# Performance work log

Hardware: AMD Instinct MI355X
Metric: run time of the kernel (lower is better)

## Reference

```python
import jax, jax.numpy as jnp
import numpy as np

N = 100_000          # nodes
E = 3_200_000        # edges (avg degree 32)
H = 20               # hidden_channels (node feature width, = 10 one-hot + 10 mlp)
EH = 64              # edge_hidden_dim
EO = 10              # edge_output_dim
THRESHOLD = 1.0


def setup_inputs() -> dict:
    key = jax.random.key(0)
    ks = jax.random.split(key, 12)
    x = jax.random.normal(ks[0], (N, 2, H), dtype=jnp.float32)
    edge_index = jax.random.randint(ks[1], (2, E), 0, N, dtype=jnp.int32)
    # distances strictly in (0, threshold]
    edge_attr = jax.random.uniform(ks[2], (E, 1), jnp.float32, 1e-4, THRESHOLD)
    # parameters (torch.rand init as in the module)
    a = jax.random.uniform(ks[3], (1,), jnp.float32)
    b = jax.random.uniform(ks[4], (1,), jnp.float32) + 1.0
    gamma1 = jax.random.uniform(ks[5], (H, H), jnp.float32)
    gamma2 = jax.random.uniform(ks[6], (H, H), jnp.float32)
    bias = jax.random.uniform(ks[7], (H,), jnp.float32)
    # edge MLP: Linear(1, EH) -> ReLU -> Linear(EH, EO)
    W1 = jax.random.normal(ks[8], (1, EH), jnp.float32)
    b1 = jnp.zeros((EH,), jnp.float32)
    W2 = jax.random.normal(ks[9], (EH, EO), jnp.float32) / np.sqrt(EH)
    b2 = jnp.zeros((EO,), jnp.float32)
    return dict(x=x, edge_index=edge_index, edge_attr=edge_attr, a=a, b=b,
                gamma1=gamma1, gamma2=gamma2, bias=bias, W1=W1, b1=b1, W2=W2, b2=b2)


def reference(x, edge_index, edge_attr, a, b, gamma1, gamma2, bias, W1, b1, W2, b2):
    src, dst = edge_index[0], edge_index[1]
    # --- edge features ---
    h = jax.nn.relu(edge_attr @ W1 + b1)            # [E, EH]
    mlp_out = h @ W2 + b2                           # [E, EO]
    # one-hot distance bucket: 10 equal intervals over (0, threshold], idx 10 -> 9
    idx = jnp.clip((edge_attr[:, 0] * (10.0 / THRESHOLD)).astype(jnp.int32), 0, 9)
    one_hot = jax.nn.one_hot(idx, 10, dtype=x.dtype)  # [E, 10]
    eac = jnp.concatenate([one_hot, mlp_out], axis=1)  # edge_attr_combined [E, 20]
    # --- per-source-node normalization (w_tilde) ---
    sum_w = jax.ops.segment_sum(eac, src, num_segments=N)  # [N, 20]
    sw = sum_w[src]                                        # [E, 20]
    safe = jnp.where(sw != 0, sw, 1.0)
    w_tilde = jnp.where(sw != 0, eac / safe, jnp.asarray(0.01, x.dtype))
    # --- rho weighting on node features ---
    h_j = x[src, 0]                                  # [E, 20]
    h_jp = x[dst, 0]                                 # [E, 20]
    rho = jnp.abs(a * h_j - (1.0 - a) * h_jp) ** b   # [E, 20]
    # --- aggregate messages per source node ---
    sum_features = jax.ops.segment_sum(rho * w_tilde, src, num_segments=N)  # [N, 20]
    # --- node update ---
    out0 = jax.nn.sigmoid(x[:, 0] @ gamma1.T + sum_features @ gamma2.T + bias)
    return jnp.stack([out0, sum_features], axis=1)   # [N, 2, 20]
```

## Files before the change

### kernel.cpp

```cpp
#include <hip/hip_runtime.h>
#include <hip/hip_bf16.h>


#define BATCH 4096
#define BPT   16
#define BSH   7
#define CAP   4608
#define GST   16

__device__ inline float blo(unsigned v) { return __uint_as_float(v << 16); }
__device__ inline float bhi(unsigned v) { return __uint_as_float(v & 0xFFFF0000u); }
__device__ inline unsigned f2bfu(float f) {
    __hip_bfloat16 h = __float2bfloat16(f);
    unsigned short us;
    __builtin_memcpy(&us, &h, 2);
    return (unsigned)us;
}

__device__ int block_scan_excl(int* data, int n, int* scratch) {
    const int t = threadIdx.x;
    const int lane = t & 63, w = t >> 6;
    const int base = t * 4;
    int v0 = (base + 0 < n) ? data[base + 0] : 0;
    int v1 = (base + 1 < n) ? data[base + 1] : 0;
    int v2 = (base + 2 < n) ? data[base + 2] : 0;
    int v3 = (base + 3 < n) ? data[base + 3] : 0;
    int p1 = v0 + v1, p2 = p1 + v2, p3 = p2 + v3;
    int x = p3;
    #pragma unroll
    for (int o = 1; o < 64; o <<= 1) { int y = __shfl_up(x, o); if (lane >= o) x += y; }
    if (lane == 63) scratch[w] = x;
    __syncthreads();
    int wbase = 0;
    for (int i = 0; i < w; ++i) wbase += scratch[i];
    int tb = wbase + x - p3;
    if (base + 0 < n) data[base + 0] = tb;
    if (base + 1 < n) data[base + 1] = tb + v0;
    if (base + 2 < n) data[base + 2] = tb + p1;
    if (base + 3 < n) data[base + 3] = tb + p2;
    int tot = scratch[0] + scratch[1] + scratch[2] + scratch[3];
    __syncthreads();
    return tot;
}

__launch_bounds__(256)
__global__ void k_scatter(const int* __restrict__ src, const int* __restrict__ dst,
                          const float* __restrict__ ea, int* __restrict__ gcursor,
                          int2* __restrict__ tmp,
                          const float* __restrict__ x, unsigned* __restrict__ xau,
                          const float* __restrict__ W1, const float* __restrict__ b1,
                          const float* __restrict__ W2, const float* __restrict__ b2,
                          float* __restrict__ AB, int* __restrict__ flag,
                          int E, int nb, int Npack, int EH, int EO) {
    __shared__ int2 pay2[BATCH];
    __shared__ int  lcount[1024];
    __shared__ int  lsave[1024];
    __shared__ int  scratch[4];
    const int t = threadIdx.x;

    if (blockIdx.x == 0) {
        if (t == 64) {
            int ok = 1;
            for (int k = 0; k < EH; ++k) if (b1[k] != 0.0f) ok = 0;
            *flag = ok;
        }
        if (t < EO) {
            float A = 0.0f;
            for (int k = 0; k < EH; ++k)
                if (W1[k] > 0.0f) A = fmaf(W1[k], W2[k * EO + t], A);
            AB[t]      = A;
            AB[EO + t] = b2[t];
        }
    }

    for (int i = t; i < 1024; i += 256) lcount[i] = 0;
    __syncthreads();
    const int base = blockIdx.x * BATCH;
    int mys[BPT], myr[BPT], myw[BPT];
    #pragma unroll
    for (int k = 0; k < BPT; ++k) {
        int e = base + k * 256 + t;
        mys[k] = -1;
        if (e < E) {
            int s = src[e], d = dst[e];
            float dd = ea[e];
            int ib = (int)(dd * 10.0f);
            ib = ib < 0 ? 0 : (ib > 9 ? 9 : ib);
            int dq = (int)fmaf(dd, 2047.0f, 0.5f);
            dq = dq < 0 ? 0 : (dq > 2047 ? 2047 : dq);
            mys[k] = s;
            myr[k] = atomicAdd(&lcount[s >> BSH], 1);
            myw[k] = (d & 0x1FFFF) | (ib << 17) | (dq << 21);
        }
    }
    __syncthreads();
    for (int i = t; i < 1024; i += 256) lsave[i] = lcount[i];
    __syncthreads();
    int total = block_scan_excl(lcount, nb, scratch);
    for (int b = t; b < nb; b += 256) {
        int c = lsave[b];
        if (c > 0) lsave[b] = atomicAdd(&gcursor[b * GST], c);
    }
    __syncthreads();
    #pragma unroll
    for (int k = 0; k < BPT; ++k) {
        if (mys[k] >= 0) {
            int b = mys[k] >> BSH;
            int pos = lcount[b] + myr[k];
            pay2[pos] = make_int2(myw[k], (b << 7) | (mys[k] & 127));
        }
    }
    __syncthreads();
    for (int j = t; j < total; j += 256) {
        int2 v = pay2[j];
        int b = v.y >> 7;
        int pos = lsave[b] + (j - lcount[b]);
        if (pos < CAP) tmp[b * CAP + pos] = v;
    }
    const int stride = gridDim.x * 256;
    for (int i = blockIdx.x * 256 + t; i < Npack * 10; i += stride) {
        int n = i / 10, p = i - n * 10;
        float2 v = *(const float2*)(x + n * 40 + p * 2);
        xau[i] = f2bfu(v.x) | (f2bfu(v.y) << 16);
    }
}

template <int USE_XA>
__launch_bounds__(512, 8)
__global__ void k_nodeb(const float* __restrict__ x,
                        const unsigned* __restrict__ xau,
                        const int* __restrict__ gcount,
                        const int2* __restrict__ tmp,
                        const float* __restrict__ a_p, const float* __restrict__ b_p,
                        const float* __restrict__ g1, const float* __restrict__ g2,
                        const float* __restrict__ bias,
                        const float* __restrict__ AB, const int* __restrict__ flag_p,
                        const float* __restrict__ W1, const float* __restrict__ b1,
                        const float* __restrict__ W2, const float* __restrict__ b2,
                        float* __restrict__ out, int N, int EH, int EO) {
    __shared__ int   buf[CAP];
    __shared__ int   hist[128];
    __shared__ int   rowstart[129];
    __shared__ int   lcur[128];
    __shared__ unsigned char perm[128];
    __shared__ __hip_bfloat16 s_x0[128 * 22];
    __shared__ float s_sf[128 * 21];
    __shared__ float s_g1[20 * 21], s_g2[20 * 21], s_b[20];

    const int t = threadIdx.x;
    const int b = blockIdx.x;
    const int node0 = b << BSH;
    const int s0 = b * CAP;
    int m = gcount[b * GST];
    if (m > CAP) m = CAP;

    if (t < 128) hist[t] = 0;
    for (int i = t; i < 400; i += 512) {
        int r = i / 20, cc = i - r * 20;
        s_g1[r * 21 + cc] = g1[i];
        s_g2[r * 21 + cc] = g2[i];
    }
    if (t < 20) s_b[t] = bias[t];
    if (USE_XA) {
        for (int i = t; i < 1280; i += 512) {
            int l = i / 10, p = i - l * 10;
            int n = node0 + l;
            unsigned v = (n < N) ? xau[n * 10 + p] : 0u;
            *(unsigned*)&s_x0[l * 22 + 2 * p] = v;
        }
    } else {
        for (int i = t; i < 2560; i += 512) {
            int l = i / 20, cc = i - l * 20;
            int n = node0 + l;
            s_x0[l * 22 + cc] = __float2bfloat16((n < N) ? x[n * 40 + cc] : 0.0f);
        }
    }
    __syncthreads();

    const int4* tw4 = (const int4*)(tmp + s0);
    int vw[10], vn[10];
    #pragma unroll
    for (int k = 0; k < 5; ++k) {
        int idx2 = k * 512 + t;
        vn[k * 2 + 0] = -1;
        vn[k * 2 + 1] = -1;
        int e0 = idx2 << 1;
        if (e0 < m) {
            int4 wv = tw4[idx2];
            vw[k * 2 + 0] = wv.x;
            vw[k * 2 + 1] = wv.z;
            { vn[k * 2 + 0] = wv.y & 127; atomicAdd(&hist[vn[k * 2 + 0]], 1); }
            if (e0 + 1 < m) { vn[k * 2 + 1] = wv.w & 127; atomicAdd(&hist[vn[k * 2 + 1]], 1); }
        }
    }
    __syncthreads();
    if (t < 64) {
        int a = hist[2 * t], bb = hist[2 * t + 1];
        int s = a + bb;
        int xsc = s;
        #pragma unroll
        for (int o = 1; o < 64; o <<= 1) { int y = __shfl_up(xsc, o); if (t >= o) xsc += y; }
        int excl = xsc - s;
        rowstart[2 * t]     = excl;
        rowstart[2 * t + 1] = excl + a;
        lcur[2 * t]         = excl;
        lcur[2 * t + 1]     = excl + a;
        if (t == 63) rowstart[128] = xsc;
    }
    __syncthreads();
    #pragma unroll
    for (int k = 0; k < 10; ++k) {
        if (vn[k] >= 0) {
            int p = atomicAdd(&lcur[vn[k]], 1);
            buf[p] = vw[k];
        }
    }
    __syncthreads();

    if (t < 128) hist[t] = 0;
    __syncthreads();
    if (t < 128) {
        int len = rowstart[t + 1] - rowstart[t];
        int bin = 127 - (len > 127 ? 127 : len);
        atomicAdd(&hist[bin], 1);
    }
    __syncthreads();
    if (t < 64) {
        int a = hist[2 * t], bb = hist[2 * t + 1];
        int s = a + bb;
        int xsc = s;
        #pragma unroll
        for (int o = 1; o < 64; o <<= 1) { int y = __shfl_up(xsc, o); if (t >= o) xsc += y; }
        int excl = xsc - s;
        hist[2 * t]     = excl;
        hist[2 * t + 1] = excl + a;
    }
    __syncthreads();
    if (t < 128) {
        int len = rowstart[t + 1] - rowstart[t];
        int bin = 127 - (len > 127 ? 127 : len);
        int pos = atomicAdd(&hist[bin], 1);
        perm[pos] = (unsigned char)t;
    }

    const float av = a_p[0], bv = b_p[0];
    const float am1 = 1.0f - av;
    const int fl = *flag_p;
    __syncthreads();

    const uint2* xg = (const uint2*)xau;
    #pragma unroll
    for (int r = 0; r < 2; ++r) {
        int item = t + 512 * r;
        if (item >= 640) break;
        int li = perm[item / 5];
        int q  = item - (item / 5) * 5;
        int c0 = q * 4;
        const bool cl0 = (c0 + 0) < 10, cl1 = (c0 + 1) < 10;
        const bool cl2 = (c0 + 2) < 10, cl3 = (c0 + 3) < 10;
        unsigned xv0 = *(const unsigned*)&s_x0[li * 22 + c0];
        unsigned xv1 = *(const unsigned*)&s_x0[li * 22 + c0 + 2];
        const float pax0 = av * blo(xv0), pax1 = av * bhi(xv0);
        const float pax2 = av * blo(xv1), pax3 = av * bhi(xv1);
        int rs = rowstart[li];
        int re = rowstart[li + 1];
        float deg = (float)(re - rs);
        float sf0, sf1, sf2, sf3;
        if (fl || (c0 + 3) < 10) {
            float sA0 = 0.f, sB0 = 0.f, s20 = 0.f;
            float sA1 = 0.f, sB1 = 0.f, s21 = 0.f;
            float sA2 = 0.f, sB2 = 0.f, s22 = 0.f;
            float sA3 = 0.f, sB3 = 0.f, s23 = 0.f;
            #pragma unroll 2
            for (int i = rs; i < re; ++i) {
                int w = buf[i];
                float xd0, xd1, xd2, xd3;
                if (USE_XA) {
                    uint2 v = xg[(unsigned)(w & 0x1FFFF) * 5u + (unsigned)q];
                    xd0 = blo(v.x); xd1 = bhi(v.x);
                    xd2 = blo(v.y); xd3 = bhi(v.y);
                } else {
                    int n = w & 0x1FFFF;
                    xd0 = x[n * 40 + c0];     xd1 = x[n * 40 + c0 + 1];
                    xd2 = x[n * 40 + c0 + 2]; xd3 = x[n * 40 + c0 + 3];
                }
                int   ib  = (w >> 17) & 0xF;
                float dqf = (float)(((unsigned)w) >> 21);
                float r0 = exp2f(bv * __log2f(fabsf(fmaf(-am1, xd0, pax0))));
                float r1 = exp2f(bv * __log2f(fabsf(fmaf(-am1, xd1, pax1))));
                float r2 = exp2f(bv * __log2f(fabsf(fmaf(-am1, xd2, pax2))));
                float r3 = exp2f(bv * __log2f(fabsf(fmaf(-am1, xd3, pax3))));
                float e0s = cl0 ? ((ib == c0)     ? 1.0f : 0.0f) : dqf;
                float e1s = cl1 ? ((ib == c0 + 1) ? 1.0f : 0.0f) : dqf;
                float e2s = cl2 ? ((ib == c0 + 2) ? 1.0f : 0.0f) : dqf;
                float e3s = cl3 ? ((ib == c0 + 3) ? 1.0f : 0.0f) : dqf;
                sA0 += e0s; sB0 = fmaf(r0, e0s, sB0); s20 += r0;
                sA1 += e1s; sB1 = fmaf(r1, e1s, sB1); s21 += r1;
                sA2 += e2s; sB2 = fmaf(r2, e2s, sB2); s22 += r2;
                sA3 += e3s; sB3 = fmaf(r3, e3s, sB3); s23 += r3;
            }
            #define FIN(K, sAk, sBk, s2k, sfk)                                     \
            {   int ck = c0 + K;                                                   \
                float sw, s1;                                                      \
                if (ck < 10) { sw = sAk; s1 = sBk; }                               \
                else { float Afq = AB[ck - 10] * (1.0f / 2047.0f);                 \
                       float Bf  = AB[ck];                                         \
                       sw = fmaf(Afq, sAk, Bf * deg);                              \
                       s1 = fmaf(Afq, sBk, Bf * s2k); }                            \
                sfk = (sw != 0.0f) ? (s1 / sw) : (0.01f * s2k);                    \
            }
            FIN(0, sA0, sB0, s20, sf0); FIN(1, sA1, sB1, s21, sf1);
            FIN(2, sA2, sB2, s22, sf2); FIN(3, sA3, sB3, s23, sf3);
            #undef FIN
        } else {
            float swk[4] = {0.f, 0.f, 0.f, 0.f};
            float s1k[4] = {0.f, 0.f, 0.f, 0.f};
            float s2k[4] = {0.f, 0.f, 0.f, 0.f};
            float paxs[4] = {pax0, pax1, pax2, pax3};
            for (int i = rs; i < re; ++i) {
                int w = buf[i];
                float xd[4];
                if (USE_XA) {
                    uint2 v = xg[(unsigned)(w & 0x1FFFF) * 5u + (unsigned)q];
                    xd[0] = blo(v.x); xd[1] = bhi(v.x);
                    xd[2] = blo(v.y); xd[3] = bhi(v.y);
                } else {
                    int n = w & 0x1FFFF;
                    #pragma unroll
                    for (int kk = 0; kk < 4; ++kk) xd[kk] = x[n * 40 + c0 + kk];
                }
                int   ib  = (w >> 17) & 0xF;
                float dd_ = (float)(((unsigned)w) >> 21) * (1.0f / 2047.0f);
                float mlp[4];
                #pragma unroll
                for (int kk = 0; kk < 4; ++kk) {
                    int ck = c0 + kk;
                    mlp[kk] = b2[ck >= 10 ? ck - 10 : 0];
                }
                for (int k_ = 0; k_ < EH; ++k_) {
                    float h_ = fmaf(dd_, W1[k_], b1[k_]);
                    h_ = h_ > 0.0f ? h_ : 0.0f;
                    #pragma unroll
                    for (int kk = 0; kk < 4; ++kk) {
                        int ck = c0 + kk;
                        mlp[kk] = fmaf(h_, W2[k_ * EO + (ck >= 10 ? ck - 10 : 0)], mlp[kk]);
                    }
                }
                #pragma unroll
                for (int kk = 0; kk < 4; ++kk) {
                    int ck = c0 + kk;
                    float rho = exp2f(bv * __log2f(fabsf(fmaf(-am1, xd[kk], paxs[kk]))));
                    float sel = (ck < 10) ? ((ib == ck) ? 1.0f : 0.0f) : mlp[kk];
                    swk[kk] += sel;
                    s1k[kk] = fmaf(rho, sel, s1k[kk]);
                    s2k[kk] += rho;
                }
            }
            sf0 = (swk[0] != 0.0f) ? (s1k[0] / swk[0]) : (0.01f * s2k[0]);
            sf1 = (swk[1] != 0.0f) ? (s1k[1] / swk[1]) : (0.01f * s2k[1]);
            sf2 = (swk[2] != 0.0f) ? (s1k[2] / swk[2]) : (0.01f * s2k[2]);
            sf3 = (swk[3] != 0.0f) ? (s1k[3] / swk[3]) : (0.01f * s2k[3]);
        }
        s_sf[li * 21 + c0]     = sf0;
        s_sf[li * 21 + c0 + 1] = sf1;
        s_sf[li * 21 + c0 + 2] = sf2;
        s_sf[li * 21 + c0 + 3] = sf3;
    }
    __syncthreads();

    for (int i = t; i < 2560; i += 512) {
        int l = i / 20, cc = i - l * 20;
        int n = node0 + l;
        if (n < N) {
            float acc = s_b[cc];
            const __hip_bfloat16* xr = &s_x0[l * 22];
            const float* sr  = &s_sf[l * 21];
            const float* g1r = &s_g1[cc * 21];
            const float* g2r = &s_g2[cc * 21];
            #pragma unroll
            for (int k = 0; k < 20; ++k)
                acc = fmaf(__bfloat162float(xr[k]), g1r[k], fmaf(sr[k], g2r[k], acc));
            float o0 = 1.0f / (1.0f + __expf(-acc));
            out[n * 40 + cc]      = o0;
            out[n * 40 + 20 + cc] = sr[cc];
        }
    }
}

extern "C" void kernel_launch(void* const* d_in, const int* in_sizes, int n_in,
                              void* d_out, int out_size, void* d_ws, size_t ws_size,
                              hipStream_t stream) {
    const float* x    = (const float*)d_in[0];
    const int*   ei   = (const int*)  d_in[1];
    const float* ea   = (const float*)d_in[2];
    const float* a_p  = (const float*)d_in[3];
    const float* b_p  = (const float*)d_in[4];
    const float* g1   = (const float*)d_in[5];
    const float* g2   = (const float*)d_in[6];
    const float* bias = (const float*)d_in[7];
    const float* W1   = (const float*)d_in[8];
    const float* b1   = (const float*)d_in[9];
    const float* W2   = (const float*)d_in[10];
    const float* b2   = (const float*)d_in[11];
    float* out = (float*)d_out;

    const int E  = in_sizes[2];
    const int N  = in_sizes[0] / 40;
    const int EH = in_sizes[8];
    const int EO = in_sizes[11];
    const int* src = ei;
    const int* dst = ei + E;

    const int nb     = (N + 127) >> BSH;
    const int nbatch = (E + BATCH - 1) / BATCH;

    char* wsb = (char*)d_ws;
    size_t o = 0;
    int* gcursor = (int*)(wsb + o); o += (size_t)nb * GST * 4;
    float* AB    = (float*)(wsb + o); o += 2 * (size_t)EO * 4;
    int* flag    = (int*)(wsb + o);   o += 4;                   o = (o + 15) & ~(size_t)15;
    int2* tmp    = (int2*)(wsb + o);  o += (size_t)nb * CAP * 8;
    unsigned* xau = (unsigned*)(wsb + o);
    const size_t need_xa = o + (size_t)N * 10 * 4;
    const int use_xa = (ws_size >= need_xa) ? 1 : 0;

    hipMemsetAsync(gcursor, 0, (size_t)nb * GST * sizeof(int), stream);

    k_scatter<<<nbatch, 256, 0, stream>>>(src, dst, ea, gcursor, tmp,
                                          x, use_xa ? xau : (unsigned*)AB,
                                          W1, b1, W2, b2, AB, flag,
                                          E, nb, use_xa ? N : 0, EH, EO);
    if (use_xa) {
        k_nodeb<1><<<nb, 512, 0, stream>>>(x, xau, gcursor, tmp, a_p, b_p,
                                           g1, g2, bias, AB, flag,
                                           W1, b1, W2, b2, out, N, EH, EO);
    } else {
        k_nodeb<0><<<nb, 512, 0, stream>>>(x, xau, gcursor, tmp, a_p, b_p,
                                           g1, g2, bias, AB, flag,
                                           W1, b1, W2, b2, out, N, EH, EO);
    }
}
```

Before: 238.9 us.

## Split per-bucket scatter cursors and segments by XCD to localize atomics

Each node bucket now gets eight sub-cursors and eight sub-segments of the staging buffer, chosen by the scatter block's index modulo 8. This targets the MI355X's separate chiplets, so global atomics and writes on a cursor stay within one chiplet's L2 instead of bouncing across dies. The node kernel reads the eight segment counts, prefix-sums them, and gathers from all sub-segments using a small search over that scan. The trade-offs are extra indexing work, a larger workspace, and a per-segment cap that can overflow and silently drop edges if one chiplet's share for a bucket is skewed.

```diff
diff --git a/kernel.cpp b/kernel.cpp
--- a/kernel.cpp
+++ b/kernel.cpp
@@ -6,6 +6,7 @@
 #define BPT   16
 #define BSH   7
 #define CAP   4608
+#define CAP8  640
 #define GST   16
 
 __device__ inline float blo(unsigned v) { return __uint_as_float(v << 16); }
@@ -57,6 +58,7 @@
     __shared__ int  lsave[1024];
     __shared__ int  scratch[4];
     const int t = threadIdx.x;
+    const int xcd = blockIdx.x & 7;
 
     if (blockIdx.x == 0) {
         if (t == 64) {
@@ -99,7 +101,7 @@
     int total = block_scan_excl(lcount, nb, scratch);
     for (int b = t; b < nb; b += 256) {
         int c = lsave[b];
-        if (c > 0) lsave[b] = atomicAdd(&gcursor[b * GST], c);
+        if (c > 0) lsave[b] = atomicAdd(&gcursor[(b * 8 + xcd) * GST], c);
     }
     __syncthreads();
     #pragma unroll
@@ -113,9 +115,9 @@
     __syncthreads();
     for (int j = t; j < total; j += 256) {
         int2 v = pay2[j];
-        int b = v.y >> 7;
-        int pos = lsave[b] + (j - lcount[b]);
-        if (pos < CAP) tmp[b * CAP + pos] = v;
+        int bb = v.y >> 7;
+        int pos = lsave[bb] + (j - lcount[bb]);
+        if (pos < CAP8) tmp[(size_t)(bb * 8 + xcd) * CAP8 + pos] = v;
     }
     const int stride = gridDim.x * 256;
     for (int i = blockIdx.x * 256 + t; i < Npack * 10; i += stride) {
@@ -143,6 +145,8 @@
     __shared__ int   rowstart[129];
     __shared__ int   lcur[128];
     __shared__ unsigned char perm[128];
+    __shared__ int   segm[8];
+    __shared__ int   cps[9];
     __shared__ __hip_bfloat16 s_x0[128 * 22];
     __shared__ float s_sf[128 * 21];
     __shared__ float s_g1[20 * 21], s_g2[20 * 21], s_b[20];
@@ -150,11 +154,18 @@
     const int t = threadIdx.x;
     const int b = blockIdx.x;
     const int node0 = b << BSH;
-    const int s0 = b * CAP;
-    int m = gcount[b * GST];
-    if (m > CAP) m = CAP;
 
     if (t < 128) hist[t] = 0;
+    if (t < 64) {
+        int c = (t < 8) ? gcount[(b * 8 + t) * GST] : 0;
+        c = c > CAP8 ? CAP8 : c;
+        int pr = (c + 1) >> 1;
+        int acc = pr;
+        #pragma unroll
+        for (int o = 1; o < 8; o <<= 1) { int y = __shfl_up(acc, o); if (t >= o) acc += y; }
+        if (t < 8) { segm[t] = c; cps[t] = acc - pr; }
+        if (t == 7) cps[8] = acc;
+    }
     for (int i = t; i < 400; i += 512) {
         int r = i / 20, cc = i - r * 20;
         s_g1[r * 21 + cc] = g1[i];
@@ -177,20 +188,26 @@
     }
     __syncthreads();
 
-    const int4* tw4 = (const int4*)(tmp + s0);
+    const int TP = cps[8];
     int vw[10], vn[10];
     #pragma unroll
     for (int k = 0; k < 5; ++k) {
-        int idx2 = k * 512 + t;
+        int pidx = k * 512 + t;
         vn[k * 2 + 0] = -1;
         vn[k * 2 + 1] = -1;
-        int e0 = idx2 << 1;
-        if (e0 < m) {
-            int4 wv = tw4[idx2];
+        if (pidx < TP) {
+            int r = 0;
+            #pragma unroll
+            for (int rr = 1; rr < 8; ++rr) if (pidx >= cps[rr]) r = rr;
+            int lp = pidx - cps[r];
+            int mr = segm[r];
+            const int4* sp = (const int4*)(tmp + (size_t)(b * 8 + r) * CAP8);
+            int4 wv = sp[lp];
+            int e0 = lp << 1;
             vw[k * 2 + 0] = wv.x;
             vw[k * 2 + 1] = wv.z;
             { vn[k * 2 + 0] = wv.y & 127; atomicAdd(&hist[vn[k * 2 + 0]], 1); }
-            if (e0 + 1 < m) { vn[k * 2 + 1] = wv.w & 127; atomicAdd(&hist[vn[k * 2 + 1]], 1); }
+            if (e0 + 1 < mr) { vn[k * 2 + 1] = wv.w & 127; atomicAdd(&hist[vn[k * 2 + 1]], 1); }
         }
     }
     __syncthreads();
@@ -212,7 +229,7 @@
     for (int k = 0; k < 10; ++k) {
         if (vn[k] >= 0) {
             int p = atomicAdd(&lcur[vn[k]], 1);
-            buf[p] = vw[k];
+            if (p < CAP) buf[p] = vw[k];
         }
     }
     __syncthreads();
@@ -416,15 +433,15 @@
 
     char* wsb = (char*)d_ws;
     size_t o = 0;
-    int* gcursor = (int*)(wsb + o); o += (size_t)nb * GST * 4;
+    int* gcursor = (int*)(wsb + o); o += (size_t)nb * 8 * GST * 4;
     float* AB    = (float*)(wsb + o); o += 2 * (size_t)EO * 4;
     int* flag    = (int*)(wsb + o);   o += 4;                   o = (o + 15) & ~(size_t)15;
-    int2* tmp    = (int2*)(wsb + o);  o += (size_t)nb * CAP * 8;
+    int2* tmp    = (int2*)(wsb + o);  o += (size_t)nb * 8 * CAP8 * 8;
     unsigned* xau = (unsigned*)(wsb + o);
     const size_t need_xa = o + (size_t)N * 10 * 4;
     const int use_xa = (ws_size >= need_xa) ? 1 : 0;
 
-    hipMemsetAsync(gcursor, 0, (size_t)nb * GST * sizeof(int), stream);
+    hipMemsetAsync(gcursor, 0, (size_t)nb * 8 * GST * sizeof(int), stream);
 
     k_scatter<<<nbatch, 256, 0, stream>>>(src, dst, ea, gcursor, tmp,
                                           x, use_xa ? xau : (unsigned*)AB,
```

Result: faster. 225.6 us (-5.6%).
